# Kernel tuning notes

Hardware: AMD Instinct MI355X
Metric: run time of the kernel (lower is better)

Reference implementation:

```python
import jax, jax.numpy as jnp
import numpy as np

N, D_IN, D_MID, D_EMB = 8192, 1024, 256, 64


def setup_inputs() -> dict:
    key = jax.random.key(0)
    k1, k2, k3, k4 = jax.random.split(key, 4)
    # scale Laplacian so repeated N x N matmuls stay numerically tame
    Laplacian = jax.random.normal(k1, (N, N), dtype=jnp.float32) / np.float32(np.sqrt(N))
    X = jax.random.normal(k2, (N, D_IN), dtype=jnp.float32)
    bound1 = np.sqrt(6.0 / (D_IN + D_MID))
    bound2 = np.sqrt(6.0 / (D_MID + D_EMB))
    W1 = jax.random.uniform(k3, (D_IN, D_MID), dtype=jnp.float32, minval=-bound1, maxval=bound1)
    W2 = jax.random.uniform(k4, (D_MID, D_EMB), dtype=jnp.float32, minval=-bound2, maxval=bound2)
    return {"Laplacian": Laplacian, "X": X, "W1": W1, "W2": W2}


def reference(Laplacian, X, W1, W2):
    # layer 1: Laplacian-smoothed linear + ReLU
    h = jax.nn.relu(Laplacian @ (X @ W1))            # [N, mid]
    # layer 2: Laplacian-smoothed linear -> embedding
    emb = Laplacian @ (h @ W2)                        # [N, emb]
    # pairwise squared Euclidean distances between embeddings (utils.distance)
    sq = jnp.sum(emb * emb, axis=1)                   # [N]
    dist = jnp.maximum(sq[:, None] + sq[None, :] - 2.0 * (emb @ emb.T), 0.0)  # [N, N]
    recons_w = jax.nn.softmax(-dist, axis=1)
    return recons_w + jnp.float32(1e-10)
```

## Files before the change

### kernel.cpp

```cpp
#include <hip/hip_runtime.h>
#include <stdint.h>

#define N_    8192
#define DIN   1024
#define DMID  256
#define DEMB  64

typedef __bf16 bf16x8 __attribute__((ext_vector_type(8)));
typedef float  f32x4  __attribute__((ext_vector_type(4)));

#define MFMA16(a, b, c) __builtin_amdgcn_mfma_f32_16x16x32_bf16((a), (b), (c), 0, 0, 0)

static __device__ __forceinline__ unsigned short f2bfu(float f) {
    union { float f; unsigned int u; } v; v.f = f;
    unsigned int r = v.u + 0x7FFFu + ((v.u >> 16) & 1u);
    return (unsigned short)(r >> 16);
}

__global__ void k_setup(const float* __restrict__ W1, const float* __restrict__ W2,
                        unsigned short* __restrict__ W1T, unsigned short* __restrict__ W2T) {
    int idx = blockIdx.x * 256 + threadIdx.x;
    if (idx < DIN * DMID) {
        int k = idx / DMID, c = idx % DMID;
        W1T[c * DIN + k] = f2bfu(W1[idx]);
    }
    int i2 = idx - DIN * DMID;
    if (i2 >= 0 && i2 < DMID * DEMB) {
        int k = i2 / DEMB, c = i2 % DEMB;
        W2T[c * DMID + k] = f2bfu(W2[i2]);
    }
}

template<int BN, int AF32, int OUTMODE, int RELU>
__global__ __launch_bounds__(512, 2)
void k_gemm(const void* __restrict__ Ag_, const unsigned short* __restrict__ Bg,
            void* __restrict__ Og, float* __restrict__ sqg,
            int K, int lda, int ldb)
{
    constexpr int NCT = BN / 64;
    const int tid  = threadIdx.x;
    const int w    = tid >> 6;
    const int lane = tid & 63;
    const int l16  = lane & 15, lhi = lane >> 4;
    const int row0 = blockIdx.x * 32;

    __shared__ __align__(16) unsigned short At[2][32 * 32];
    __shared__ __align__(16) unsigned short Bt[2][BN * 32];
    __shared__ float sql[32];

    if (OUTMODE == 2 && tid < 32) sql[tid] = 0.0f;

    const float*          Af = (const float*)Ag_;
    const unsigned short* Ah = (const unsigned short*)Ag_;

    const int s_arow = tid >> 4;
    const int s_ak   = (tid & 15) * 2;

    f32x4 acc[NCT];
    #pragma unroll
    for (int i = 0; i < NCT; ++i) { f32x4 z = {0.f, 0.f, 0.f, 0.f}; acc[i] = z; }

    float2  arf; ushort2 arh; uint4 brg[2];
    const int NT = K >> 5;

    auto stage_load = [&](int t) {
        int k0 = t << 5;
        if (AF32) {
            union { double d; float2 f; } cvt;
            cvt.d = __builtin_nontemporal_load(
                (const double*)&Af[(size_t)(row0 + s_arow) * lda + k0 + s_ak]);
            arf = cvt.f;
        } else {
            arh = *(const ushort2*)&Ah[(size_t)(row0 + s_arow) * lda + k0 + s_ak];
        }
        if (BN == 256) {
            #pragma unroll
            for (int i = 0; i < 2; ++i) {
                int u = tid + i * 512;
                int col = u >> 2, ks = (u & 3) * 8;
                brg[i] = *(const uint4*)&Bg[(size_t)col * ldb + k0 + ks];
            }
        } else {
            if (tid < 256) {
                int col = tid >> 2, ks = (tid & 3) * 8;
                brg[0] = *(const uint4*)&Bg[(size_t)col * ldb + k0 + ks];
            }
        }
    };
    auto stage_write = [&](int buf) {
        {
            ushort2 o;
            if (AF32) { o.x = f2bfu(arf.x); o.y = f2bfu(arf.y); }
            else      { o = arh; }
            int e = (s_arow * 32 + s_ak) ^ ((s_arow & 7) << 3);
            *(ushort2*)&At[buf][e] = o;
        }
        if (BN == 256) {
            #pragma unroll
            for (int i = 0; i < 2; ++i) {
                int u = tid + i * 512;
                int col = u >> 2, ks = (u & 3) * 8;
                int e = (col * 32 + ks) ^ ((col & 7) << 3);
                *(uint4*)&Bt[buf][e] = brg[i];
            }
        } else {
            if (tid < 256) {
                int col = tid >> 2, ks = (tid & 3) * 8;
                int e = (col * 32 + ks) ^ ((col & 7) << 3);
                *(uint4*)&Bt[buf][e] = brg[0];
            }
        }
    };

    stage_load(0);
    stage_write(0);
    __syncthreads();

    const int a_r   = 16 * (w & 1) + l16;
    const int a_off = (a_r * 32 + lhi * 8) ^ ((a_r & 7) << 3);

    for (int t = 0; t < NT; ++t) {
        int cur = t & 1;
        if (t + 1 < NT) stage_load(t + 1);
        bf16x8 a = *(const bf16x8*)&At[cur][a_off];
        #pragma unroll
        for (int ct = 0; ct < NCT; ++ct) {
            int col = ((w >> 1) * NCT + ct) * 16 + l16;
            int e = (col * 32 + lhi * 8) ^ ((col & 7) << 3);
            bf16x8 b = *(const bf16x8*)&Bt[cur][e];
            acc[ct] = MFMA16(a, b, acc[ct]);
        }
        __syncthreads();
        if (t + 1 < NT) {
            stage_write(cur ^ 1);
            __syncthreads();
        }
    }

    if (OUTMODE == 0) {
        unsigned short* OT = (unsigned short*)Og;
        int rowb = row0 + 16 * (w & 1) + lhi * 4;
        #pragma unroll
        for (int ct = 0; ct < NCT; ++ct) {
            int col = ((w >> 1) * NCT + ct) * 16 + l16;
            ushort4 o;
            o.x = f2bfu(acc[ct][0]); o.y = f2bfu(acc[ct][1]);
            o.z = f2bfu(acc[ct][2]); o.w = f2bfu(acc[ct][3]);
            *(ushort4*)&OT[(size_t)col * N_ + rowb] = o;
        }
    } else {
        unsigned short* O = (unsigned short*)Og;
        float sp[4] = {0.f, 0.f, 0.f, 0.f};
        #pragma unroll
        for (int ct = 0; ct < NCT; ++ct) {
            int col = ((w >> 1) * NCT + ct) * 16 + l16;
            #pragma unroll
            for (int i = 0; i < 4; ++i) {
                int row = row0 + 16 * (w & 1) + lhi * 4 + i;
                float v = acc[ct][i];
                if (RELU) v = fmaxf(v, 0.f);
                unsigned short u = f2bfu(v);
                O[(size_t)row * BN + col] = u;
                if (OUTMODE == 2) {
                    union { unsigned int ui; float f; } cv; cv.ui = (unsigned int)u << 16;
                    sp[i] += cv.f * cv.f;
                }
            }
        }
        if (OUTMODE == 2) {
            #pragma unroll
            for (int off = 1; off < 16; off <<= 1) {
                #pragma unroll
                for (int i = 0; i < 4; ++i) sp[i] += __shfl_xor(sp[i], off);
            }
            if (l16 == 0) {
                #pragma unroll
                for (int i = 0; i < 4; ++i)
                    atomicAdd(&sql[16 * (w & 1) + lhi * 4 + i], sp[i]);
            }
            __syncthreads();
            if (tid < 32) sqg[row0 + tid] = sql[tid];
        }
    }
    (void)sqg;
}

__global__ __launch_bounds__(512, 2)
void k_softmax(const unsigned short* __restrict__ embb, const float* __restrict__ sq,
               float* __restrict__ out)
{
    const int tid  = threadIdx.x;
    const int w    = tid >> 6;
    const int lane = tid & 63;
    const int l16  = lane & 15, lhi = lane >> 4;
    const int row0 = blockIdx.x * 32;

    __shared__ float red_s[8][32];
    __shared__ float srow[32];

    bf16x8 afr[2][2];
    #pragma unroll
    for (int tr = 0; tr < 2; ++tr)
        #pragma unroll
        for (int ks = 0; ks < 2; ++ks)
            afr[tr][ks] = *(const bf16x8*)&embb[(size_t)(row0 + 16 * tr + l16) * 64 + ks * 32 + lhi * 8];

    float sqr[2][4];
    #pragma unroll
    for (int tr = 0; tr < 2; ++tr)
        #pragma unroll
        for (int i = 0; i < 4; ++i)
            sqr[tr][i] = sq[row0 + 16 * tr + lhi * 4 + i];

    const int colw0 = w * 1024;

    float s_[2][4] = {{0.f,0.f,0.f,0.f},{0.f,0.f,0.f,0.f}};

    for (int ch = 0; ch < 16; ++ch) {
        int cb = colw0 + ch * 64;
        #pragma unroll
        for (int ct = 0; ct < 4; ++ct) {
            int col = cb + ct * 16 + l16;
            bf16x8 b0 = *(const bf16x8*)&embb[(size_t)col * 64 + lhi * 8];
            bf16x8 b1 = *(const bf16x8*)&embb[(size_t)col * 64 + 32 + lhi * 8];
            float sqc = sq[col];
            #pragma unroll
            for (int tr = 0; tr < 2; ++tr) {
                f32x4 g = {0.f, 0.f, 0.f, 0.f};
                g = MFMA16(afr[tr][0], b0, g);
                g = MFMA16(afr[tr][1], b1, g);
                #pragma unroll
                for (int i = 0; i < 4; ++i) {
                    float nd = fminf(__builtin_fmaf(2.0f, g[i], -(sqr[tr][i] + sqc)), 0.0f);
                    s_[tr][i] += __expf(nd);
                }
            }
        }
    }

    #pragma unroll
    for (int off = 1; off < 16; off <<= 1) {
        #pragma unroll
        for (int tr = 0; tr < 2; ++tr)
            #pragma unroll
            for (int i = 0; i < 4; ++i)
                s_[tr][i] += __shfl_xor(s_[tr][i], off);
    }
    if (l16 == 0) {
        #pragma unroll
        for (int tr = 0; tr < 2; ++tr)
            #pragma unroll
            for (int i = 0; i < 4; ++i)
                red_s[w][16 * tr + lhi * 4 + i] = s_[tr][i];
    }
    __syncthreads();
    if (tid < 32) {
        float s = red_s[0][tid];
        #pragma unroll
        for (int j = 1; j < 8; ++j) s += red_s[j][tid];
        srow[tid] = 1.0f / s;
    }
    __syncthreads();
    float rsloc[2][4];
    #pragma unroll
    for (int tr = 0; tr < 2; ++tr)
        #pragma unroll
        for (int i = 0; i < 4; ++i)
            rsloc[tr][i] = srow[16 * tr + lhi * 4 + i];

    for (int ch = 0; ch < 16; ++ch) {
        int cb = colw0 + ch * 64;
        #pragma unroll
        for (int ct = 0; ct < 4; ++ct) {
            int col = cb + ct * 16 + l16;
            bf16x8 b0 = *(const bf16x8*)&embb[(size_t)col * 64 + lhi * 8];
            bf16x8 b1 = *(const bf16x8*)&embb[(size_t)col * 64 + 32 + lhi * 8];
            float sqc = sq[col];
            #pragma unroll
            for (int tr = 0; tr < 2; ++tr) {
                f32x4 g = {0.f, 0.f, 0.f, 0.f};
                g = MFMA16(afr[tr][0], b0, g);
                g = MFMA16(afr[tr][1], b1, g);
                #pragma unroll
                for (int i = 0; i < 4; ++i) {
                    float nd = fminf(__builtin_fmaf(2.0f, g[i], -(sqr[tr][i] + sqc)), 0.0f);
                    float p = __expf(nd) * rsloc[tr][i] + 1e-10f;
                    int row = row0 + 16 * tr + lhi * 4 + i;
                    __builtin_nontemporal_store(p, &out[(size_t)row * N_ + col]);
                }
            }
        }
    }
}

extern "C" void kernel_launch(void* const* d_in, const int* in_sizes, int n_in,
                              void* d_out, int out_size, void* d_ws, size_t ws_size,
                              hipStream_t stream)
{
    const float* L  = (const float*)d_in[0];
    const float* X  = (const float*)d_in[1];
    const float* W1 = (const float*)d_in[2];
    const float* W2 = (const float*)d_in[3];
    float* out = (float*)d_out;
    char* ws = (char*)d_ws;

    unsigned short* AT  = (unsigned short*)(ws);
    unsigned short* Hh  = (unsigned short*)(ws + (4ll  << 20));
    unsigned short* PT  = (unsigned short*)(ws + (8ll  << 20));
    unsigned short* EB  = (unsigned short*)(ws + (9ll  << 20));
    float*          SQ  = (float*)         (ws + (10ll << 20));
    unsigned short* W1T = (unsigned short*)(ws + (11ll << 20));
    unsigned short* W2T = (unsigned short*)(ws + (11ll << 20) + (512ll << 10));

    k_setup<<<(DIN * DMID + DMID * DEMB + 255) / 256, 256, 0, stream>>>(W1, W2, W1T, W2T);

    k_gemm<256, 1, 0, 0><<<256, 512, 0, stream>>>(X,  W1T, AT, nullptr, DIN,  DIN,  DIN);
    k_gemm<256, 1, 1, 1><<<256, 512, 0, stream>>>(L,  AT,  Hh, nullptr, N_,   N_,   N_);
    k_gemm< 64, 0, 0, 0><<<256, 512, 0, stream>>>(Hh, W2T, PT, nullptr, DMID, DMID, DMID);
    k_gemm< 64, 1, 2, 0><<<256, 512, 0, stream>>>(L,  PT,  EB, SQ,      N_,   N_,   N_);
    k_softmax<<<256, 512, 0, stream>>>(EB, SQ, out);
}
```

Before: 1.231 ms.

## Deepen GEMM prefetch to two stages and halve softmax rows per block

The GEMM main loop now holds two register staging sets, so global loads for tiles t+3 and t+4 are issued while the current tile computes. This hides more global-memory latency at the cost of more registers. The softmax kernel now handles 16 rows per block instead of 32 and launches 512 blocks. Its column loop is software-pipelined with double-buffered register loads of the embedding columns. Halving rows per block doubles the per-row reuse of each loaded column fragment's cost but adds parallelism across blocks.

```diff
diff --git a/kernel.cpp b/kernel.cpp
--- a/kernel.cpp
+++ b/kernel.cpp
@@ -60,38 +60,40 @@
     #pragma unroll
     for (int i = 0; i < NCT; ++i) { f32x4 z = {0.f, 0.f, 0.f, 0.f}; acc[i] = z; }
 
-    float2  arf; ushort2 arh; uint4 brg[2];
     const int NT = K >> 5;
 
-    auto stage_load = [&](int t) {
+    struct SReg { float2 arf; ushort2 arh; uint4 brg[2]; };
+    SReg sa, sb;
+
+    auto ld = [&](SReg& r, int t) {
         int k0 = t << 5;
         if (AF32) {
             union { double d; float2 f; } cvt;
             cvt.d = __builtin_nontemporal_load(
                 (const double*)&Af[(size_t)(row0 + s_arow) * lda + k0 + s_ak]);
-            arf = cvt.f;
+            r.arf = cvt.f;
         } else {
-            arh = *(const ushort2*)&Ah[(size_t)(row0 + s_arow) * lda + k0 + s_ak];
+            r.arh = *(const ushort2*)&Ah[(size_t)(row0 + s_arow) * lda + k0 + s_ak];
         }
         if (BN == 256) {
             #pragma unroll
             for (int i = 0; i < 2; ++i) {
                 int u = tid + i * 512;
                 int col = u >> 2, ks = (u & 3) * 8;
-                brg[i] = *(const uint4*)&Bg[(size_t)col * ldb + k0 + ks];
+                r.brg[i] = *(const uint4*)&Bg[(size_t)col * ldb + k0 + ks];
             }
         } else {
             if (tid < 256) {
                 int col = tid >> 2, ks = (tid & 3) * 8;
-                brg[0] = *(const uint4*)&Bg[(size_t)col * ldb + k0 + ks];
-            }
-        }
-    };
-    auto stage_write = [&](int buf) {
+                r.brg[0] = *(const uint4*)&Bg[(size_t)col * ldb + k0 + ks];
+            }
+        }
+    };
+    auto st = [&](int buf, SReg& r) {
         {
             ushort2 o;
-            if (AF32) { o.x = f2bfu(arf.x); o.y = f2bfu(arf.y); }
-            else      { o = arh; }
+            if (AF32) { o.x = f2bfu(r.arf.x); o.y = f2bfu(r.arf.y); }
+            else      { o = r.arh; }
             int e = (s_arow * 32 + s_ak) ^ ((s_arow & 7) << 3);
             *(ushort2*)&At[buf][e] = o;
         }
@@ -101,27 +103,21 @@
                 int u = tid + i * 512;
                 int col = u >> 2, ks = (u & 3) * 8;
                 int e = (col * 32 + ks) ^ ((col & 7) << 3);
-                *(uint4*)&Bt[buf][e] = brg[i];
+                *(uint4*)&Bt[buf][e] = r.brg[i];
             }
         } else {
             if (tid < 256) {
                 int col = tid >> 2, ks = (tid & 3) * 8;
                 int e = (col * 32 + ks) ^ ((col & 7) << 3);
-                *(uint4*)&Bt[buf][e] = brg[0];
-            }
-        }
-    };
-
-    stage_load(0);
-    stage_write(0);
-    __syncthreads();
+                *(uint4*)&Bt[buf][e] = r.brg[0];
+            }
+        }
+    };
 
     const int a_r   = 16 * (w & 1) + l16;
     const int a_off = (a_r * 32 + lhi * 8) ^ ((a_r & 7) << 3);
 
-    for (int t = 0; t < NT; ++t) {
-        int cur = t & 1;
-        if (t + 1 < NT) stage_load(t + 1);
+    auto mm = [&](int cur) {
         bf16x8 a = *(const bf16x8*)&At[cur][a_off];
         #pragma unroll
         for (int ct = 0; ct < NCT; ++ct) {
@@ -130,9 +126,25 @@
             bf16x8 b = *(const bf16x8*)&Bt[cur][e];
             acc[ct] = MFMA16(a, b, acc[ct]);
         }
+    };
+
+    ld(sa, 0);
+    st(0, sa);
+    ld(sa, 1);
+    ld(sb, 2);
+    __syncthreads();
+
+    for (int t = 0; t < NT; t += 2) {
+        mm(0);
         __syncthreads();
-        if (t + 1 < NT) {
-            stage_write(cur ^ 1);
+        st(1, sa);
+        if (t + 3 < NT) ld(sa, t + 3);
+        __syncthreads();
+        mm(1);
+        __syncthreads();
+        if (t + 2 < NT) {
+            st(0, sb);
+            if (t + 4 < NT) ld(sb, t + 4);
             __syncthreads();
         }
     }
@@ -193,102 +205,100 @@
     const int w    = tid >> 6;
     const int lane = tid & 63;
     const int l16  = lane & 15, lhi = lane >> 4;
-    const int row0 = blockIdx.x * 32;
-
-    __shared__ float red_s[8][32];
-    __shared__ float srow[32];
-
-    bf16x8 afr[2][2];
-    #pragma unroll
-    for (int tr = 0; tr < 2; ++tr)
-        #pragma unroll
-        for (int ks = 0; ks < 2; ++ks)
-            afr[tr][ks] = *(const bf16x8*)&embb[(size_t)(row0 + 16 * tr + l16) * 64 + ks * 32 + lhi * 8];
-
-    float sqr[2][4];
-    #pragma unroll
-    for (int tr = 0; tr < 2; ++tr)
+    const int row0 = blockIdx.x * 16;
+
+    __shared__ float red_s[8][16];
+    __shared__ float srow[16];
+
+    bf16x8 afr[2];
+    #pragma unroll
+    for (int ks = 0; ks < 2; ++ks)
+        afr[ks] = *(const bf16x8*)&embb[(size_t)(row0 + l16) * 64 + ks * 32 + lhi * 8];
+
+    float sqr[4];
+    #pragma unroll
+    for (int i = 0; i < 4; ++i)
+        sqr[i] = sq[row0 + lhi * 4 + i];
+
+    const int colw0 = w * 1024;
+
+    auto ldc = [&](int cc, bf16x8& b0, bf16x8& b1, float& sc) {
+        int col = colw0 + cc * 16 + l16;
+        b0 = *(const bf16x8*)&embb[(size_t)col * 64 + lhi * 8];
+        b1 = *(const bf16x8*)&embb[(size_t)col * 64 + 32 + lhi * 8];
+        sc = sq[col];
+    };
+
+    float s_[4] = {0.f, 0.f, 0.f, 0.f};
+
+    auto procA = [&](bf16x8 b0, bf16x8 b1, float sqc) {
+        f32x4 g = {0.f, 0.f, 0.f, 0.f};
+        g = MFMA16(afr[0], b0, g);
+        g = MFMA16(afr[1], b1, g);
+        #pragma unroll
+        for (int i = 0; i < 4; ++i) {
+            float nd = fminf(__builtin_fmaf(2.0f, g[i], -(sqr[i] + sqc)), 0.0f);
+            s_[i] += __expf(nd);
+        }
+    };
+
+    {
+        bf16x8 b0a, b1a, b0b, b1b; float sca, scb;
+        ldc(0, b0a, b1a, sca);
+        for (int cc = 0; cc < 64; cc += 2) {
+            ldc(cc + 1, b0b, b1b, scb);
+            procA(b0a, b1a, sca);
+            if (cc + 2 < 64) ldc(cc + 2, b0a, b1a, sca);
+            procA(b0b, b1b, scb);
+        }
+    }
+
+    #pragma unroll
+    for (int off = 1; off < 16; off <<= 1) {
         #pragma unroll
         for (int i = 0; i < 4; ++i)
-            sqr[tr][i] = sq[row0 + 16 * tr + lhi * 4 + i];
-
-    const int colw0 = w * 1024;
-
-    float s_[2][4] = {{0.f,0.f,0.f,0.f},{0.f,0.f,0.f,0.f}};
-
-    for (int ch = 0; ch < 16; ++ch) {
-        int cb = colw0 + ch * 64;
-        #pragma unroll
-        for (int ct = 0; ct < 4; ++ct) {
-            int col = cb + ct * 16 + l16;
-            bf16x8 b0 = *(const bf16x8*)&embb[(size_t)col * 64 + lhi * 8];
-            bf16x8 b1 = *(const bf16x8*)&embb[(size_t)col * 64 + 32 + lhi * 8];
-            float sqc = sq[col];
-            #pragma unroll
-            for (int tr = 0; tr < 2; ++tr) {
-                f32x4 g = {0.f, 0.f, 0.f, 0.f};
-                g = MFMA16(afr[tr][0], b0, g);
-                g = MFMA16(afr[tr][1], b1, g);
-                #pragma unroll
-                for (int i = 0; i < 4; ++i) {
-                    float nd = fminf(__builtin_fmaf(2.0f, g[i], -(sqr[tr][i] + sqc)), 0.0f);
-                    s_[tr][i] += __expf(nd);
-                }
-            }
-        }
-    }
-
-    #pragma unroll
-    for (int off = 1; off < 16; off <<= 1) {
-        #pragma unroll
-        for (int tr = 0; tr < 2; ++tr)
-            #pragma unroll
-            for (int i = 0; i < 4; ++i)
-                s_[tr][i] += __shfl_xor(s_[tr][i], off);
+            s_[i] += __shfl_xor(s_[i], off);
     }
     if (l16 == 0) {
         #pragma unroll
-        for (int tr = 0; tr < 2; ++tr)
-            #pragma unroll
-            for (int i = 0; i < 4; ++i)
-                red_s[w][16 * tr + lhi * 4 + i] = s_[tr][i];
+        for (int i = 0; i < 4; ++i)
+            red_s[w][lhi * 4 + i] = s_[i];
     }
     __syncthreads();
-    if (tid < 32) {
+    if (tid < 16) {
         float s = red_s[0][tid];
         #pragma unroll
         for (int j = 1; j < 8; ++j) s += red_s[j][tid];
         srow[tid] = 1.0f / s;
     }
     __syncthreads();
-    float rsloc[2][4];
-    #pragma unroll
-    for (int tr = 0; tr < 2; ++tr)
-        #pragma unroll
-        for (int i = 0; i < 4; ++i)
-            rsloc[tr][i] = srow[16 * tr + lhi * 4 + i];
-
-    for (int ch = 0; ch < 16; ++ch) {
-        int cb = colw0 + ch * 64;
-        #pragma unroll
-        for (int ct = 0; ct < 4; ++ct) {
-            int col = cb + ct * 16 + l16;
-            bf16x8 b0 = *(const bf16x8*)&embb[(size_t)col * 64 + lhi * 8];
-            bf16x8 b1 = *(const bf16x8*)&embb[(size_t)col * 64 + 32 + lhi * 8];
-            float sqc = sq[col];
-            #pragma unroll
-            for (int tr = 0; tr < 2; ++tr) {
-                f32x4 g = {0.f, 0.f, 0.f, 0.f};
-                g = MFMA16(afr[tr][0], b0, g);
-                g = MFMA16(afr[tr][1], b1, g);
-                #pragma unroll
-                for (int i = 0; i < 4; ++i) {
-                    float nd = fminf(__builtin_fmaf(2.0f, g[i], -(sqr[tr][i] + sqc)), 0.0f);
-                    float p = __expf(nd) * rsloc[tr][i] + 1e-10f;
-                    int row = row0 + 16 * tr + lhi * 4 + i;
-                    __builtin_nontemporal_store(p, &out[(size_t)row * N_ + col]);
-                }
-            }
+    float rsloc[4];
+    #pragma unroll
+    for (int i = 0; i < 4; ++i)
+        rsloc[i] = srow[lhi * 4 + i];
+
+    auto procB = [&](int cc, bf16x8 b0, bf16x8 b1, float sqc) {
+        f32x4 g = {0.f, 0.f, 0.f, 0.f};
+        g = MFMA16(afr[0], b0, g);
+        g = MFMA16(afr[1], b1, g);
+        int col = colw0 + cc * 16 + l16;
+        #pragma unroll
+        for (int i = 0; i < 4; ++i) {
+            float nd = fminf(__builtin_fmaf(2.0f, g[i], -(sqr[i] + sqc)), 0.0f);
+            float p = __expf(nd) * rsloc[i] + 1e-10f;
+            int row = row0 + lhi * 4 + i;
+            __builtin_nontemporal_store(p, &out[(size_t)row * N_ + col]);
+        }
+    };
+
+    {
+        bf16x8 b0a, b1a, b0b, b1b; float sca, scb;
+        ldc(0, b0a, b1a, sca);
+        for (int cc = 0; cc < 64; cc += 2) {
+            ldc(cc + 1, b0b, b1b, scb);
+            procB(cc, b0a, b1a, sca);
+            if (cc + 2 < 64) ldc(cc + 2, b0a, b1a, sca);
+            procB(cc + 1, b0b, b1b, scb);
         }
     }
 }
@@ -318,5 +328,5 @@
     k_gemm<256, 1, 1, 1><<<256, 512, 0, stream>>>(L,  AT,  Hh, nullptr, N_,   N_,   N_);
     k_gemm< 64, 0, 0, 0><<<256, 512, 0, stream>>>(Hh, W2T, PT, nullptr, DMID, DMID, DMID);
     k_gemm< 64, 1, 2, 0><<<256, 512, 0, stream>>>(L,  PT,  EB, SQ,      N_,   N_,   N_);
-    k_softmax<<<256, 512, 0, stream>>>(EB, SQ, out);
-}
+    k_softmax<<<512, 512, 0, stream>>>(EB, SQ, out);
+}
```

Result: faster. 1.120 ms (-9.0%).
